# Optimization experiments

Measured on AMD Instinct MI355X. Metric: run time of the kernel, lower is better.

The kernel has to match this reference:

```python
import jax, jax.numpy as jnp
import numpy as np
import math

H = 128      # hidden_size
B = 4        # bsz
N = 32       # bsz * num_doc_per_q
L = 128      # doc_len


def setup_inputs() -> dict:
    key = jax.random.key(0)
    ks = jax.random.split(key, 7)
    word_ent_info = jax.random.normal(ks[0], (N, L, H), dtype=jnp.float32)
    word_ent_info_mask = jax.random.randint(ks[1], (N, L), 0, 2, dtype=jnp.int32)
    doc = jax.random.normal(ks[2], (N, L, H), dtype=jnp.float32)
    doc_mask = jax.random.randint(ks[3], (N, L), 0, 2, dtype=jnp.int32)
    q_for_text = jax.random.normal(ks[4], (B, H), dtype=jnp.float32)
    # nn.Linear(3H, H): weight [H, 3H], bias [H]
    W1 = jax.random.normal(ks[5], (H, 3 * H), dtype=jnp.float32) / math.sqrt(3 * H)
    b1 = jnp.zeros((H,), dtype=jnp.float32)
    # nn.Linear(H, 1): weight [1, H], bias [1]
    w2 = jax.random.normal(ks[6], (1, H), dtype=jnp.float32) / math.sqrt(H)
    b2 = jnp.zeros((1,), dtype=jnp.float32)
    return {"word_ent_info": word_ent_info, "word_ent_info_mask": word_ent_info_mask,
            "doc": doc, "doc_mask": doc_mask, "q_for_text": q_for_text,
            "W1": W1, "b1": b1, "w2": w2, "b2": b2}


def reference(word_ent_info, word_ent_info_mask, doc, doc_mask, q_for_text, W1, b1, w2, b2):
    n, l, h = doc.shape
    bsz = q_for_text.shape[0]
    dt = doc.dtype

    # word_ent_infoagg = mask^T @ word_ent_info -> [N, H]
    m = word_ent_info_mask.astype(dt)
    ent_agg = jnp.einsum('nl,nlh->nh', m, word_ent_info)

    # q expanded to one row per document: [N, H]
    q_exp = jnp.repeat(q_for_text, n // bsz, axis=0)

    # Split W1 over the concat([doc_self, ent_agg, q_agg]) feature axis.
    # score_pre[n,j,k,:] = W1a @ (doc_j*doc_k) + W1b @ (doc_j*ent_agg) + W1c @ (doc_k*q)
    W1a, W1b, W1c = jnp.split(W1, 3, axis=1)        # each [H, H]
    A = jnp.einsum('nje,nke,ge->njkg', doc, doc, W1a)          # [N,L,L,H]
    Bt = jnp.einsum('nje,ge->njg', doc * ent_agg[:, None, :], W1b)  # [N,L,H]
    Ct = jnp.einsum('nke,ge->nkg', doc * q_exp[:, None, :], W1c)    # [N,L,H]
    hid = jnp.tanh(A + Bt[:, :, None, :] + Ct[:, None, :, :] + b1)  # [N,L,L,H]

    score = (jnp.einsum('njkg,g->njk', hid, w2[0]) + b2[0]) / math.sqrt(h)

    dm = doc_mask.astype(dt)
    score_mask = dm[:, :, None] * dm[:, None, :]     # [N,L,L]
    score = jnp.where(score_mask == 0.0, jnp.asarray(-1e9, dt), score)
    w = jax.nn.softmax(score, axis=-1) * score_mask
    doc_ent_enc = jnp.einsum('njk,nkh->njh', w, doc)  # [N,L,H]
    return doc_ent_enc
```

## Files before the change

### kernel.cpp

```cpp
#include <hip/hip_runtime.h>
#include <hip/hip_bf16.h>
#include <math.h>

#define Hh 128
#define Nn 32
#define Ll 128
#define W1S 384
#define PAD 136

typedef __attribute__((ext_vector_type(8))) short short8;
typedef __attribute__((ext_vector_type(4))) float floatx4;

__device__ __forceinline__ unsigned short f2bf(float x) {
  __hip_bfloat16 h = __float2bfloat16(x);
  return __builtin_bit_cast(unsigned short, h);
}
__device__ __forceinline__ float bf2f(short s) {
  unsigned int u = ((unsigned int)(unsigned short)s) << 16;
  return __builtin_bit_cast(float, u);
}
__device__ __forceinline__ short8 pack8(float4 a, float4 b) {
  short8 r;
  r[0] = (short)f2bf(a.x); r[1] = (short)f2bf(a.y);
  r[2] = (short)f2bf(a.z); r[3] = (short)f2bf(a.w);
  r[4] = (short)f2bf(b.x); r[5] = (short)f2bf(b.y);
  r[6] = (short)f2bf(b.z); r[7] = (short)f2bf(b.w);
  return r;
}

__launch_bounds__(256, 1)
__global__ void k_prep(const float* __restrict__ wei, const int* __restrict__ wmask,
                       const float* __restrict__ doc, const float* __restrict__ q,
                       const float* __restrict__ W1,
                       float* __restrict__ Bt, float* __restrict__ Ct) {
  __shared__ __align__(16) short docb[Hh * PAD];
  __shared__ __align__(16) short Wb[Hh * PAD];
  __shared__ __align__(16) short Wc[Hh * PAD];
  __shared__ __align__(16) float entL[Hh];
  __shared__ __align__(16) float qL[Hh];
  __shared__ __align__(16) float red[2][Hh];

  int n = blockIdx.x, tid = threadIdx.x;
  const float* docn = doc + (size_t)n * Ll * Hh;
  int e8 = (tid & 15) * 8;

#pragma unroll
  for (int p = 0; p < 8; ++p) {
    int row = p * 16 + (tid >> 4);
    const float4* dp = (const float4*)(docn + (size_t)row * Hh + e8);
    *(short8*)(docb + row * PAD + e8) = pack8(dp[0], dp[1]);
    const float4* wbp = (const float4*)(W1 + (size_t)row * W1S + Hh + e8);
    *(short8*)(Wb + row * PAD + e8) = pack8(wbp[0], wbp[1]);
    const float4* wcp = (const float4*)(W1 + (size_t)row * W1S + 2 * Hh + e8);
    *(short8*)(Wc + row * PAD + e8) = pack8(wcp[0], wcp[1]);
  }
  {
    int e = tid & 127, half = tid >> 7;
    const float* wp = wei + (size_t)n * Ll * Hh + (size_t)half * 64 * Hh + e;
    const int* mp = wmask + n * Ll + half * 64;
    float a = 0.f;
#pragma unroll 8
    for (int l = 0; l < 64; ++l) a = fmaf((float)mp[l], wp[(size_t)l * Hh], a);
    red[half][e] = a;
  }
  if (tid < Hh) qL[tid] = q[(n >> 3) * Hh + tid];
  __syncthreads();
  if (tid < Hh) entL[tid] = red[0][tid] + red[1][tid];
  __syncthreads();

  int lane = tid & 63, w = tid >> 6;
  int l15 = lane & 15, quad = lane >> 4;

  float ef[32], qf[32];
#pragma unroll
  for (int c = 0; c < 4; ++c)
#pragma unroll
    for (int i = 0; i < 8; ++i) {
      int e = c * 32 + quad * 8 + i;
      ef[c * 8 + i] = entL[e];
      qf[c * 8 + i] = qL[e];
    }
  short8 draw[2][4];
#pragma unroll
  for (int mt = 0; mt < 2; ++mt)
#pragma unroll
    for (int c = 0; c < 4; ++c)
      draw[mt][c] = *(const short8*)(docb + (w * 32 + mt * 16 + l15) * PAD + c * 32 + quad * 8);

  for (int which = 0; which < 2; ++which) {
    const short* Ws = which ? Wc : Wb;
    const float* sf = which ? qf : ef;
    floatx4 acc[2][8];
#pragma unroll
    for (int mt = 0; mt < 2; ++mt)
#pragma unroll
      for (int nt = 0; nt < 8; ++nt) acc[mt][nt] = (floatx4){0.f, 0.f, 0.f, 0.f};
#pragma unroll
    for (int c = 0; c < 4; ++c) {
      short8 af[2];
#pragma unroll
      for (int mt = 0; mt < 2; ++mt) {
        float t[8];
#pragma unroll
        for (int i = 0; i < 8; ++i) t[i] = bf2f(draw[mt][c][i]) * sf[c * 8 + i];
        short8 r;
#pragma unroll
        for (int i = 0; i < 8; ++i) r[i] = (short)f2bf(t[i]);
        af[mt] = r;
      }
      short8 bfr[8];
#pragma unroll
      for (int nt = 0; nt < 8; ++nt)
        bfr[nt] = *(const short8*)(Ws + (nt * 16 + l15) * PAD + c * 32 + quad * 8);
#pragma unroll
      for (int mt = 0; mt < 2; ++mt)
#pragma unroll
        for (int nt = 0; nt < 8; ++nt)
          acc[mt][nt] = __builtin_amdgcn_mfma_f32_16x16x32_bf16(af[mt], bfr[nt], acc[mt][nt], 0, 0, 0);
    }
    float* outp = (which ? Ct : Bt) + (size_t)n * Ll * Hh;
#pragma unroll
    for (int mt = 0; mt < 2; ++mt)
#pragma unroll
      for (int nt = 0; nt < 8; ++nt)
#pragma unroll
        for (int r = 0; r < 4; ++r) {
          int k = w * 32 + mt * 16 + quad * 4 + r;
          outp[(size_t)k * Hh + nt * 16 + l15] = acc[mt][nt][r];
        }
  }
}

__launch_bounds__(256, 2)
__global__ void k_main(const float* __restrict__ doc, const int* __restrict__ dmask,
                       const float* __restrict__ W1, const float* __restrict__ b1,
                       const float* __restrict__ w2, const float* __restrict__ b2,
                       const float* __restrict__ Bt, const float* __restrict__ Ct,
                       float* __restrict__ out) {
  __shared__ __align__(16) short As[Hh * PAD];
  __shared__ __align__(16) short Bs[Hh * PAD];
  __shared__ __align__(16) float sc[Ll];
  __shared__ __align__(16) float scw[Ll];

  int bid = blockIdx.x;
  int n = bid & 31, j = bid >> 5;
  int tid = threadIdx.x;
  const float* docn = doc + (size_t)n * Ll * Hh;
  size_t orow = ((size_t)n * Ll + j) * Hh;

  if (dmask[n * Ll + j] == 0) {
    if (tid < Hh) out[orow + tid] = 0.f;
    return;
  }

  int e8 = (tid & 15) * 8;
  const float4* jp = (const float4*)(docn + (size_t)j * Hh + e8);
  float4 j0 = jp[0], j1 = jp[1];
#pragma unroll
  for (int p = 0; p < 8; ++p) {
    int row = p * 16 + (tid >> 4);
    const float4* wp = (const float4*)(W1 + (size_t)row * W1S + e8);
    *(short8*)(As + row * PAD + e8) = pack8(wp[0], wp[1]);
    const float4* dp = (const float4*)(docn + (size_t)row * Hh + e8);
    float4 d0 = dp[0], d1 = dp[1];
    d0.x *= j0.x; d0.y *= j0.y; d0.z *= j0.z; d0.w *= j0.w;
    d1.x *= j1.x; d1.y *= j1.y; d1.z *= j1.z; d1.w *= j1.w;
    *(short8*)(Bs + row * PAD + e8) = pack8(d0, d1);
  }
  __syncthreads();

  int lane = tid & 63, w = tid >> 6;
  int l15 = lane & 15, quad = lane >> 4;
  floatx4 acc[2][8];
#pragma unroll
  for (int mt = 0; mt < 2; ++mt)
#pragma unroll
    for (int nt = 0; nt < 8; ++nt) acc[mt][nt] = (floatx4){0.f, 0.f, 0.f, 0.f};
#pragma unroll
  for (int e0 = 0; e0 < Hh; e0 += 32) {
    int eo = e0 + quad * 8;
    short8 af[2], bfr[8];
    af[0] = *(const short8*)(Bs + (w * 32 + l15) * PAD + eo);
    af[1] = *(const short8*)(Bs + (w * 32 + 16 + l15) * PAD + eo);
#pragma unroll
    for (int nt = 0; nt < 8; ++nt)
      bfr[nt] = *(const short8*)(As + (nt * 16 + l15) * PAD + eo);
#pragma unroll
    for (int mt = 0; mt < 2; ++mt)
#pragma unroll
      for (int nt = 0; nt < 8; ++nt)
        acc[mt][nt] = __builtin_amdgcn_mfma_f32_16x16x32_bf16(af[mt], bfr[nt], acc[mt][nt], 0, 0, 0);
  }

  const float c2 = 2.885390081777927f;
  float bbc[8], w2r[8];
  const float* btrow = Bt + orow;
#pragma unroll
  for (int nt = 0; nt < 8; ++nt) {
    int g = nt * 16 + l15;
    bbc[nt] = (btrow[g] + b1[g]) * c2;
    w2r[nt] = w2[g];
  }
  const float* ctn = Ct + (size_t)n * Ll * Hh;
#pragma unroll
  for (int mt = 0; mt < 2; ++mt) {
#pragma unroll
    for (int r = 0; r < 4; ++r) {
      int k = w * 32 + mt * 16 + quad * 4 + r;
      const float* ctp = ctn + (size_t)k * Hh + l15;
      float p = 0.f;
#pragma unroll
      for (int nt = 0; nt < 8; ++nt) {
        float s = acc[mt][nt][r] + ctp[nt * 16];
        float a2 = fmaf(s, c2, bbc[nt]);
        float e = exp2f(a2);
        float th = fmaf(-2.f, __builtin_amdgcn_rcpf(e + 1.f), 1.f);
        p = fmaf(th, w2r[nt], p);
      }
      p += __shfl_xor(p, 1);
      p += __shfl_xor(p, 2);
      p += __shfl_xor(p, 4);
      p += __shfl_xor(p, 8);
      if (l15 == 0) sc[k] = p;
    }
  }
  __syncthreads();

  {
    float b2v = b2[0];
    const float inv = 0.088388347648318447f;
    const int* dmn = dmask + n * Ll;
    int m0 = dmn[lane], m1 = dmn[lane + 64];
    float s0 = (sc[lane] + b2v) * inv;
    float s1 = (sc[lane + 64] + b2v) * inv;
    s0 = m0 ? s0 : -1e9f;
    s1 = m1 ? s1 : -1e9f;
    float mx = fmaxf(s0, s1);
#pragma unroll
    for (int off = 32; off; off >>= 1) mx = fmaxf(mx, __shfl_xor(mx, off));
    float ex0 = __expf(s0 - mx), ex1 = __expf(s1 - mx);
    float sm = ex0 + ex1;
#pragma unroll
    for (int off = 32; off; off >>= 1) sm += __shfl_xor(sm, off);
    float rden = 1.f / sm;
    scw[lane] = m0 ? ex0 * rden : 0.f;
    scw[lane + 64] = m1 ? ex1 * rden : 0.f;
  }
  __syncthreads();

  float* ored = (float*)As;
  int half = tid >> 7, h = tid & 127;
  const float* dbase = docn + (size_t)half * 64 * Hh + h;
  float o = 0.f;
#pragma unroll 8
  for (int kk = 0; kk < 64; ++kk)
    o = fmaf(scw[half * 64 + kk], dbase[(size_t)kk * Hh], o);
  ored[half * Hh + h] = o;
  __syncthreads();
  if (tid < Ll) out[orow + tid] = ored[tid] + ored[Hh + tid];
}

extern "C" void kernel_launch(void* const* d_in, const int* in_sizes, int n_in,
                              void* d_out, int out_size, void* d_ws, size_t ws_size,
                              hipStream_t stream) {
  const float* wei   = (const float*)d_in[0];
  const int*   wmask = (const int*)d_in[1];
  const float* doc   = (const float*)d_in[2];
  const int*   dmask = (const int*)d_in[3];
  const float* q     = (const float*)d_in[4];
  const float* W1    = (const float*)d_in[5];
  const float* b1    = (const float*)d_in[6];
  const float* w2    = (const float*)d_in[7];
  const float* b2    = (const float*)d_in[8];
  float* out = (float*)d_out;

  float* ws = (float*)d_ws;
  float* Bt = ws;
  float* Ct = Bt + (size_t)Nn * Ll * Hh;

  k_prep<<<Nn, 256, 0, stream>>>(wei, wmask, doc, q, W1, Bt, Ct);
  k_main<<<Nn * Ll, 256, 0, stream>>>(doc, dmask, W1, b1, w2, b2, Bt, Ct, out);
}
```

Before: 135.8 us.

## Split prep kernel across more blocks and widen main kernel to 512 threads

The prep kernel now launches four blocks per document, one per (Bt/Ct, row-half) pair instead of one block doing everything, and folds b1 into Bt. Each block stages only its own weight slice and scales doc in fp32 before the bf16 cast. The main kernel moves to 512 threads so each wave owns one 16-row MFMA tile, and the final weighted sum is split four ways. The aim is more parallelism and lower per-thread register pressure in both kernels. The cost is that the W1 tile staging is repeated across more threads and an extra reduction step is added.

```diff
diff --git a/kernel.cpp b/kernel.cpp
--- a/kernel.cpp
+++ b/kernel.cpp
@@ -28,112 +28,99 @@
   return r;
 }
 
-__launch_bounds__(256, 1)
+__launch_bounds__(256, 2)
 __global__ void k_prep(const float* __restrict__ wei, const int* __restrict__ wmask,
                        const float* __restrict__ doc, const float* __restrict__ q,
-                       const float* __restrict__ W1,
+                       const float* __restrict__ W1, const float* __restrict__ b1,
                        float* __restrict__ Bt, float* __restrict__ Ct) {
-  __shared__ __align__(16) short docb[Hh * PAD];
-  __shared__ __align__(16) short Wb[Hh * PAD];
-  __shared__ __align__(16) short Wc[Hh * PAD];
-  __shared__ __align__(16) float entL[Hh];
-  __shared__ __align__(16) float qL[Hh];
+  __shared__ __align__(16) short Wsb[Hh * PAD];
+  __shared__ __align__(16) short docb[64 * PAD];
   __shared__ __align__(16) float red[2][Hh];
-
-  int n = blockIdx.x, tid = threadIdx.x;
+  __shared__ __align__(16) float scale[Hh];
+
+  int b = blockIdx.x;
+  int n = b >> 2, which = (b >> 1) & 1, mh = b & 1;
+  int tid = threadIdx.x;
   const float* docn = doc + (size_t)n * Ll * Hh;
   int e8 = (tid & 15) * 8;
 
+  float4 dreg[4][2];
+#pragma unroll
+  for (int p = 0; p < 4; ++p) {
+    int row = mh * 64 + p * 16 + (tid >> 4);
+    const float4* dp = (const float4*)(docn + (size_t)row * Hh + e8);
+    dreg[p][0] = dp[0]; dreg[p][1] = dp[1];
+  }
 #pragma unroll
   for (int p = 0; p < 8; ++p) {
     int row = p * 16 + (tid >> 4);
-    const float4* dp = (const float4*)(docn + (size_t)row * Hh + e8);
-    *(short8*)(docb + row * PAD + e8) = pack8(dp[0], dp[1]);
-    const float4* wbp = (const float4*)(W1 + (size_t)row * W1S + Hh + e8);
-    *(short8*)(Wb + row * PAD + e8) = pack8(wbp[0], wbp[1]);
-    const float4* wcp = (const float4*)(W1 + (size_t)row * W1S + 2 * Hh + e8);
-    *(short8*)(Wc + row * PAD + e8) = pack8(wcp[0], wcp[1]);
-  }
+    const float4* wp = (const float4*)(W1 + (size_t)row * W1S + (which + 1) * Hh + e8);
+    *(short8*)(Wsb + row * PAD + e8) = pack8(wp[0], wp[1]);
+  }
+  if (which == 1) {
+    if (tid < Hh) scale[tid] = q[(n >> 3) * Hh + tid];
+  } else {
+    int e = tid & 127, halfl = tid >> 7;
+    const float* wp = wei + (size_t)n * Ll * Hh + (size_t)halfl * 64 * Hh + e;
+    const int* mp = wmask + n * Ll + halfl * 64;
+    float a = 0.f;
+#pragma unroll 16
+    for (int l = 0; l < 64; ++l) a = fmaf((float)mp[l], wp[(size_t)l * Hh], a);
+    red[halfl][e] = a;
+  }
+  __syncthreads();
+  if (which == 0 && tid < Hh) scale[tid] = red[0][tid] + red[1][tid];
+  __syncthreads();
+
   {
-    int e = tid & 127, half = tid >> 7;
-    const float* wp = wei + (size_t)n * Ll * Hh + (size_t)half * 64 * Hh + e;
-    const int* mp = wmask + n * Ll + half * 64;
-    float a = 0.f;
-#pragma unroll 8
-    for (int l = 0; l < 64; ++l) a = fmaf((float)mp[l], wp[(size_t)l * Hh], a);
-    red[half][e] = a;
-  }
-  if (tid < Hh) qL[tid] = q[(n >> 3) * Hh + tid];
-  __syncthreads();
-  if (tid < Hh) entL[tid] = red[0][tid] + red[1][tid];
+    float s[8];
+#pragma unroll
+    for (int i = 0; i < 8; ++i) s[i] = scale[e8 + i];
+#pragma unroll
+    for (int p = 0; p < 4; ++p) {
+      int r = p * 16 + (tid >> 4);
+      float4 a = dreg[p][0], bq = dreg[p][1];
+      a.x *= s[0]; a.y *= s[1]; a.z *= s[2]; a.w *= s[3];
+      bq.x *= s[4]; bq.y *= s[5]; bq.z *= s[6]; bq.w *= s[7];
+      *(short8*)(docb + r * PAD + e8) = pack8(a, bq);
+    }
+  }
   __syncthreads();
 
   int lane = tid & 63, w = tid >> 6;
   int l15 = lane & 15, quad = lane >> 4;
-
-  float ef[32], qf[32];
-#pragma unroll
-  for (int c = 0; c < 4; ++c)
-#pragma unroll
-    for (int i = 0; i < 8; ++i) {
-      int e = c * 32 + quad * 8 + i;
-      ef[c * 8 + i] = entL[e];
-      qf[c * 8 + i] = qL[e];
+  floatx4 acc[8];
+#pragma unroll
+  for (int nt = 0; nt < 8; ++nt) acc[nt] = (floatx4){0.f, 0.f, 0.f, 0.f};
+#pragma unroll
+  for (int c = 0; c < 4; ++c) {
+    int eo = c * 32 + quad * 8;
+    short8 af = *(const short8*)(docb + (w * 16 + l15) * PAD + eo);
+    short8 bfr[8];
+#pragma unroll
+    for (int nt = 0; nt < 8; ++nt)
+      bfr[nt] = *(const short8*)(Wsb + (nt * 16 + l15) * PAD + eo);
+#pragma unroll
+    for (int nt = 0; nt < 8; ++nt)
+      acc[nt] = __builtin_amdgcn_mfma_f32_16x16x32_bf16(af, bfr[nt], acc[nt], 0, 0, 0);
+  }
+
+  float* outp = (which ? Ct : Bt) + (size_t)n * Ll * Hh;
+#pragma unroll
+  for (int nt = 0; nt < 8; ++nt) {
+    int g = nt * 16 + l15;
+    float badd = which ? 0.f : b1[g];
+#pragma unroll
+    for (int r = 0; r < 4; ++r) {
+      int k = mh * 64 + w * 16 + quad * 4 + r;
+      outp[(size_t)k * Hh + g] = acc[nt][r] + badd;
     }
-  short8 draw[2][4];
-#pragma unroll
-  for (int mt = 0; mt < 2; ++mt)
-#pragma unroll
-    for (int c = 0; c < 4; ++c)
-      draw[mt][c] = *(const short8*)(docb + (w * 32 + mt * 16 + l15) * PAD + c * 32 + quad * 8);
-
-  for (int which = 0; which < 2; ++which) {
-    const short* Ws = which ? Wc : Wb;
-    const float* sf = which ? qf : ef;
-    floatx4 acc[2][8];
-#pragma unroll
-    for (int mt = 0; mt < 2; ++mt)
-#pragma unroll
-      for (int nt = 0; nt < 8; ++nt) acc[mt][nt] = (floatx4){0.f, 0.f, 0.f, 0.f};
-#pragma unroll
-    for (int c = 0; c < 4; ++c) {
-      short8 af[2];
-#pragma unroll
-      for (int mt = 0; mt < 2; ++mt) {
-        float t[8];
-#pragma unroll
-        for (int i = 0; i < 8; ++i) t[i] = bf2f(draw[mt][c][i]) * sf[c * 8 + i];
-        short8 r;
-#pragma unroll
-        for (int i = 0; i < 8; ++i) r[i] = (short)f2bf(t[i]);
-        af[mt] = r;
-      }
-      short8 bfr[8];
-#pragma unroll
-      for (int nt = 0; nt < 8; ++nt)
-        bfr[nt] = *(const short8*)(Ws + (nt * 16 + l15) * PAD + c * 32 + quad * 8);
-#pragma unroll
-      for (int mt = 0; mt < 2; ++mt)
-#pragma unroll
-        for (int nt = 0; nt < 8; ++nt)
-          acc[mt][nt] = __builtin_amdgcn_mfma_f32_16x16x32_bf16(af[mt], bfr[nt], acc[mt][nt], 0, 0, 0);
-    }
-    float* outp = (which ? Ct : Bt) + (size_t)n * Ll * Hh;
-#pragma unroll
-    for (int mt = 0; mt < 2; ++mt)
-#pragma unroll
-      for (int nt = 0; nt < 8; ++nt)
-#pragma unroll
-        for (int r = 0; r < 4; ++r) {
-          int k = w * 32 + mt * 16 + quad * 4 + r;
-          outp[(size_t)k * Hh + nt * 16 + l15] = acc[mt][nt][r];
-        }
-  }
-}
-
-__launch_bounds__(256, 2)
+  }
+}
+
+__launch_bounds__(512, 4)
 __global__ void k_main(const float* __restrict__ doc, const int* __restrict__ dmask,
-                       const float* __restrict__ W1, const float* __restrict__ b1,
+                       const float* __restrict__ W1,
                        const float* __restrict__ w2, const float* __restrict__ b2,
                        const float* __restrict__ Bt, const float* __restrict__ Ct,
                        float* __restrict__ out) {
@@ -157,8 +144,8 @@
   const float4* jp = (const float4*)(docn + (size_t)j * Hh + e8);
   float4 j0 = jp[0], j1 = jp[1];
 #pragma unroll
-  for (int p = 0; p < 8; ++p) {
-    int row = p * 16 + (tid >> 4);
+  for (int p = 0; p < 4; ++p) {
+    int row = p * 32 + (tid >> 4);
     const float4* wp = (const float4*)(W1 + (size_t)row * W1S + e8);
     *(short8*)(As + row * PAD + e8) = pack8(wp[0], wp[1]);
     const float4* dp = (const float4*)(docn + (size_t)row * Hh + e8);
@@ -171,26 +158,6 @@
 
   int lane = tid & 63, w = tid >> 6;
   int l15 = lane & 15, quad = lane >> 4;
-  floatx4 acc[2][8];
-#pragma unroll
-  for (int mt = 0; mt < 2; ++mt)
-#pragma unroll
-    for (int nt = 0; nt < 8; ++nt) acc[mt][nt] = (floatx4){0.f, 0.f, 0.f, 0.f};
-#pragma unroll
-  for (int e0 = 0; e0 < Hh; e0 += 32) {
-    int eo = e0 + quad * 8;
-    short8 af[2], bfr[8];
-    af[0] = *(const short8*)(Bs + (w * 32 + l15) * PAD + eo);
-    af[1] = *(const short8*)(Bs + (w * 32 + 16 + l15) * PAD + eo);
-#pragma unroll
-    for (int nt = 0; nt < 8; ++nt)
-      bfr[nt] = *(const short8*)(As + (nt * 16 + l15) * PAD + eo);
-#pragma unroll
-    for (int mt = 0; mt < 2; ++mt)
-#pragma unroll
-      for (int nt = 0; nt < 8; ++nt)
-        acc[mt][nt] = __builtin_amdgcn_mfma_f32_16x16x32_bf16(af[mt], bfr[nt], acc[mt][nt], 0, 0, 0);
-  }
 
   const float c2 = 2.885390081777927f;
   float bbc[8], w2r[8];
@@ -198,31 +165,45 @@
 #pragma unroll
   for (int nt = 0; nt < 8; ++nt) {
     int g = nt * 16 + l15;
-    bbc[nt] = (btrow[g] + b1[g]) * c2;
+    bbc[nt] = btrow[g] * c2;
     w2r[nt] = w2[g];
   }
+
+  floatx4 acc[8];
+#pragma unroll
+  for (int nt = 0; nt < 8; ++nt) acc[nt] = (floatx4){0.f, 0.f, 0.f, 0.f};
+#pragma unroll
+  for (int e0 = 0; e0 < Hh; e0 += 32) {
+    int eo = e0 + quad * 8;
+    short8 af = *(const short8*)(Bs + (w * 16 + l15) * PAD + eo);
+    short8 bfr[8];
+#pragma unroll
+    for (int nt = 0; nt < 8; ++nt)
+      bfr[nt] = *(const short8*)(As + (nt * 16 + l15) * PAD + eo);
+#pragma unroll
+    for (int nt = 0; nt < 8; ++nt)
+      acc[nt] = __builtin_amdgcn_mfma_f32_16x16x32_bf16(af, bfr[nt], acc[nt], 0, 0, 0);
+  }
+
   const float* ctn = Ct + (size_t)n * Ll * Hh;
 #pragma unroll
-  for (int mt = 0; mt < 2; ++mt) {
-#pragma unroll
-    for (int r = 0; r < 4; ++r) {
-      int k = w * 32 + mt * 16 + quad * 4 + r;
-      const float* ctp = ctn + (size_t)k * Hh + l15;
-      float p = 0.f;
-#pragma unroll
-      for (int nt = 0; nt < 8; ++nt) {
-        float s = acc[mt][nt][r] + ctp[nt * 16];
-        float a2 = fmaf(s, c2, bbc[nt]);
-        float e = exp2f(a2);
-        float th = fmaf(-2.f, __builtin_amdgcn_rcpf(e + 1.f), 1.f);
-        p = fmaf(th, w2r[nt], p);
-      }
-      p += __shfl_xor(p, 1);
-      p += __shfl_xor(p, 2);
-      p += __shfl_xor(p, 4);
-      p += __shfl_xor(p, 8);
-      if (l15 == 0) sc[k] = p;
+  for (int r = 0; r < 4; ++r) {
+    int k = w * 16 + quad * 4 + r;
+    const float* ctp = ctn + (size_t)k * Hh + l15;
+    float p = 0.f;
+#pragma unroll
+    for (int nt = 0; nt < 8; ++nt) {
+      float s = acc[nt][r] + ctp[nt * 16];
+      float a2 = fmaf(s, c2, bbc[nt]);
+      float e = exp2f(a2);
+      float th = fmaf(-2.f, __builtin_amdgcn_rcpf(e + 1.f), 1.f);
+      p = fmaf(th, w2r[nt], p);
     }
+    p += __shfl_xor(p, 1);
+    p += __shfl_xor(p, 2);
+    p += __shfl_xor(p, 4);
+    p += __shfl_xor(p, 8);
+    if (l15 == 0) sc[k] = p;
   }
   __syncthreads();
 
@@ -249,15 +230,16 @@
   __syncthreads();
 
   float* ored = (float*)As;
-  int half = tid >> 7, h = tid & 127;
-  const float* dbase = docn + (size_t)half * 64 * Hh + h;
+  int halfk = tid >> 7, h = tid & 127;
+  const float* dbase = docn + (size_t)halfk * 32 * Hh + h;
   float o = 0.f;
 #pragma unroll 8
-  for (int kk = 0; kk < 64; ++kk)
-    o = fmaf(scw[half * 64 + kk], dbase[(size_t)kk * Hh], o);
-  ored[half * Hh + h] = o;
-  __syncthreads();
-  if (tid < Ll) out[orow + tid] = ored[tid] + ored[Hh + tid];
+  for (int kk = 0; kk < 32; ++kk)
+    o = fmaf(scw[halfk * 32 + kk], dbase[(size_t)kk * Hh], o);
+  ored[halfk * Hh + h] = o;
+  __syncthreads();
+  if (tid < Ll)
+    out[orow + tid] = ored[tid] + ored[Hh + tid] + ored[2 * Hh + tid] + ored[3 * Hh + tid];
 }
 
 extern "C" void kernel_launch(void* const* d_in, const int* in_sizes, int n_in,
@@ -278,6 +260,6 @@
   float* Bt = ws;
   float* Ct = Bt + (size_t)Nn * Ll * Hh;
 
-  k_prep<<<Nn, 256, 0, stream>>>(wei, wmask, doc, q, W1, Bt, Ct);
-  k_main<<<Nn * Ll, 256, 0, stream>>>(doc, dmask, W1, b1, w2, b2, Bt, Ct, out);
-}
+  k_prep<<<Nn * 4, 256, 0, stream>>>(wei, wmask, doc, q, W1, b1, Bt, Ct);
+  k_main<<<Nn * Ll, 512, 0, stream>>>(doc, dmask, W1, w2, b2, Bt, Ct, out);
+}
```

Result: faster. 123.8 us (-8.8%).
